# Kernel optimization log

Measured on AMD Instinct MI355X. Metric: run time of the kernel, lower is better.

Reference implementation:

```python
import jax, jax.numpy as jnp
import numpy as np

B, D, H, W, C = 2, 128, 128, 128, 4
OD, OH, OW = 96, 96, 96
RANK = 3


def setup_inputs() -> dict:
    key = jax.random.key(0)
    k1, k2 = jax.random.split(key)
    inputs = jax.random.normal(k1, (B, D, H, W, C), dtype=jnp.float32)
    # continuous sample coords in [0, size-1] per spatial dim
    scale = jnp.array([D - 1, H - 1, W - 1], dtype=jnp.float32)
    sample_coords = jax.random.uniform(k2, (B, OD, OH, OW, RANK), dtype=jnp.float32) * scale
    return {"inputs": inputs, "sample_coords": sample_coords}


def _pyramid_combination(samples, w_0, w_1):
    # recursive weighted blend over 2^rank corner samples (matches TF module)
    if len(w_0) == 1:
        return samples[0] * w_1[0] + samples[1] * w_0[0]
    f_0 = _pyramid_combination(samples[::2], w_0[:-1], w_1[:-1])
    f_1 = _pyramid_combination(samples[1::2], w_0[:-1], w_1[:-1])
    return f_0 * w_1[-1] + f_1 * w_0[-1]


def reference(inputs, sample_coords):
    # inputs: [B, D, H, W, C]; sample_coords: [B, od, oh, ow, 3]
    in_spatial = inputs.shape[1:-1]
    rank = len(in_spatial)
    batch = inputs.shape[0]

    coords = [sample_coords[..., d] for d in range(rank)]          # each [B, od, oh, ow]
    base = [jnp.floor(c) for c in coords]
    # ZERO boundary -> replicate clamp of integer coords
    floor_i = [jnp.clip(b.astype(jnp.int32), 0, in_spatial[d] - 1) for d, b in enumerate(base)]
    ceil_i = [jnp.clip((b + 1.0).astype(jnp.int32), 0, in_spatial[d] - 1) for d, b in enumerate(base)]

    # ZERO-boundary weights use the CLAMPED corner coords (faithful to source)
    w_0 = [(c - f.astype(jnp.float32))[..., None] for c, f in zip(coords, floor_i)]
    w_1 = [(ce.astype(jnp.float32) - c)[..., None] for c, ce in zip(coords, ceil_i)]

    bids = jnp.arange(batch)[:, None, None, None]                  # broadcast batch ids
    sc = (floor_i, ceil_i)

    samples = []
    for i in range(2 ** rank):
        bits = [(i >> (rank - 1 - d)) & 1 for d in range(rank)]    # dim-0 is most significant bit
        idx = [sc[bits[d]][d] for d in range(rank)]
        samples.append(inputs[bids, idx[0], idx[1], idx[2]])       # [B, od, oh, ow, C]

    return _pyramid_combination(samples, w_0, w_1)
```

## Files before the change

kernel.cpp:

```cpp
#include <hip/hip_runtime.h>
#include <hip/hip_fp16.h>


constexpr int D = 128, H = 128, W = 128;
constexpr int OD = 96, OH = 96, OW = 96;
constexpr int VOX_PER_B = OD * OH * OW;
constexpr int NVOX = 2 * VOX_PER_B;

constexpr int NBINS = 1024;
constexpr int CAP = 2048;
constexpr int NB1 = 216;
constexpr int SPB = 8192;
constexpr int GT = 1024;
constexpr int TILE_ELEMS = 9 * 5 * 128;

struct Rec { unsigned w0, w1, w2; };

constexpr size_t OFF_GCNT    = 0;
constexpr size_t OFF_RECORDS = 4096;
constexpr size_t WS_REQUIRED = OFF_RECORDS + (size_t)NBINS * CAP * 12;

__device__ __forceinline__ float4 f4_fma(float w, float4 a, float4 acc) {
    acc.x = fmaf(w, a.x, acc.x);
    acc.y = fmaf(w, a.y, acc.y);
    acc.z = fmaf(w, a.z, acc.z);
    acc.w = fmaf(w, a.w, acc.w);
    return acc;
}
__device__ __forceinline__ float4 f4_scale(float w, float4 a) {
    return make_float4(w * a.x, w * a.y, w * a.z, w * a.w);
}

__device__ __forceinline__ float4 xblend(uint2 p0, uint2 p1, float w0, float w1) {
    const __half2 a0 = *(const __half2*)&p0.x;
    const __half2 a1 = *(const __half2*)&p0.y;
    const __half2 b0 = *(const __half2*)&p1.x;
    const __half2 b1 = *(const __half2*)&p1.y;
    const float2 A0 = __half22float2(a0), A1 = __half22float2(a1);
    const float2 B0 = __half22float2(b0), B1 = __half22float2(b1);
    float4 o;
    o.x = fmaf(w1, B0.x, w0 * A0.x);
    o.y = fmaf(w1, B0.y, w0 * A0.y);
    o.z = fmaf(w1, B1.x, w0 * A1.x);
    o.w = fmaf(w1, B1.y, w0 * A1.y);
    return o;
}

__device__ __forceinline__ float4 trilinear(const float* __restrict__ inp,
                                            float cz, float cy, float cx, int b) {
    const int fz = (int)floorf(cz);
    const int fy = (int)floorf(cy);
    const int fx = (int)floorf(cx);
    const int z1 = min(max(fz + 1, 0), D - 1);
    const int y1 = min(max(fy + 1, 0), H - 1);
    const int x1 = min(max(fx + 1, 0), W - 1);
    const int z0 = min(max(fz, 0), D - 1);
    const int y0 = min(max(fy, 0), H - 1);
    const int x0 = min(max(fx, 0), W - 1);
    const float wz0 = (float)z1 - cz, wz1 = cz - (float)z0;
    const float wy0 = (float)y1 - cy, wy1 = cy - (float)y0;
    const float wx0 = (float)x1 - cx, wx1 = cx - (float)x0;
    const float4* bp = (const float4*)inp + ((size_t)b << 21);
    const int z0o = z0 << 14, z1o = z1 << 14;
    const int y0o = y0 << 7,  y1o = y1 << 7;
    const float4 s000 = bp[z0o | y0o | x0];
    const float4 s001 = bp[z0o | y0o | x1];
    const float4 s010 = bp[z0o | y1o | x0];
    const float4 s011 = bp[z0o | y1o | x1];
    const float4 s100 = bp[z1o | y0o | x0];
    const float4 s101 = bp[z1o | y0o | x1];
    const float4 s110 = bp[z1o | y1o | x0];
    const float4 s111 = bp[z1o | y1o | x1];
    float4 c00 = f4_fma(wx1, s001, f4_scale(wx0, s000));
    float4 c01 = f4_fma(wx1, s011, f4_scale(wx0, s010));
    float4 c10 = f4_fma(wx1, s101, f4_scale(wx0, s100));
    float4 c11 = f4_fma(wx1, s111, f4_scale(wx0, s110));
    float4 c0 = f4_fma(wy1, c01, f4_scale(wy0, c00));
    float4 c1 = f4_fma(wy1, c11, f4_scale(wy0, c10));
    return f4_fma(wz1, c1, f4_scale(wz0, c0));
}

__global__ __launch_bounds__(1024) void fused_scatter_kernel(
    const float* __restrict__ coords,
    const float* __restrict__ inp,
    unsigned* __restrict__ gcnt,
    Rec* __restrict__ records,
    float4* __restrict__ out)
{
    __shared__ Rec rec[SPB];
    __shared__ unsigned short binid[SPB];
    __shared__ unsigned cnt[NBINS];
    __shared__ unsigned pref[NBINS];
    __shared__ unsigned gb[NBINS];
    __shared__ unsigned s[1024];
    const int t = threadIdx.x;
    cnt[t] = 0;
    __syncthreads();

    const int s0 = blockIdx.x * SPB;
    unsigned w0r[8], w1r[8], w2r[8], rankr[8];
    int kr[8];
#pragma unroll
    for (int j = 0; j < 8; j++) {
        const int smp = s0 + j * 1024 + t;
        const float cz = coords[smp * 3 + 0];
        const float cy = coords[smp * 3 + 1];
        const float cx = coords[smp * 3 + 2];
        const int b = (smp >= VOX_PER_B) ? 1 : 0;
        const int z0 = (int)floorf(cz);
        const int y0 = (int)floorf(cy);
        const int x0 = (int)floorf(cx);
        const unsigned fzq = min((unsigned)((cz - (float)z0) * 65536.0f), 65535u);
        const unsigned fyq = min((unsigned)((cy - (float)y0) * 65536.0f), 65535u);
        const unsigned fxq = min((unsigned)((cx - (float)x0) * 65536.0f), 65535u);
        const int k = (b << 9) | ((z0 >> 3) << 5) | (y0 >> 2);
        kr[j] = k;
        w0r[j] = (unsigned)smp | ((unsigned)(z0 & 7) << 21) | ((unsigned)(y0 & 3) << 24);
        w1r[j] = fzq | (fyq << 16);
        w2r[j] = fxq | ((unsigned)x0 << 16);
        rankr[j] = atomicAdd(&cnt[k], 1u);
    }
    __syncthreads();

    pref[t] = cnt[t];
    __syncthreads();
    for (int off = 1; off < NBINS; off <<= 1) {
        unsigned u = (t >= off) ? pref[t - off] : 0u;
        __syncthreads();
        pref[t] += u;
        __syncthreads();
    }
    {
        unsigned ex = pref[t] - cnt[t];
        __syncthreads();
        pref[t] = ex;
    }
    gb[t] = atomicAdd(&gcnt[t], cnt[t]);
    __syncthreads();

#pragma unroll
    for (int j = 0; j < 8; j++) {
        const unsigned slot = pref[kr[j]] + rankr[j];
        rec[slot].w0 = w0r[j];
        rec[slot].w1 = w1r[j];
        rec[slot].w2 = w2r[j];
        binid[slot] = (unsigned short)kr[j];
    }
    __syncthreads();

#pragma unroll
    for (int j = 0; j < 8; j++) {
        const int i = j * 1024 + t;
        const int k = binid[i];
        const unsigned pos = gb[k] + (unsigned)(i - (int)pref[k]);
        const Rec r = rec[i];
        if (pos < (unsigned)CAP) {
            records[(size_t)k * CAP + pos] = r;
        } else {
            const unsigned idx = r.w0 & 0x1FFFFFu;
            const int b  = k >> 9;
            const int z0 = ((k >> 5) & 15) * 8 + (int)((r.w0 >> 21) & 7u);
            const int y0 = (k & 31) * 4 + (int)((r.w0 >> 24) & 3u);
            const int x0 = (int)(r.w2 >> 16) & 127;
            const float cz = (float)z0 + (float)(r.w1 & 0xFFFFu) * (1.0f / 65536.0f);
            const float cy = (float)y0 + (float)(r.w1 >> 16) * (1.0f / 65536.0f);
            const float cx = (float)x0 + (float)(r.w2 & 0xFFFFu) * (1.0f / 65536.0f);
            out[idx] = trilinear(inp, cz, cy, cx, b);
        }
    }
}

__device__ __forceinline__ void blend_store(const uint2* __restrict__ tile,
                                            const Rec r, float4* __restrict__ out) {
    const unsigned idx = r.w0 & 0x1FFFFFu;
    const int z0l = (int)((r.w0 >> 21) & 7u);
    const int y0l = (int)((r.w0 >> 24) & 3u);
    const int x0  = (int)(r.w2 >> 16) & 127;
    const float wz1 = (float)(r.w1 & 0xFFFFu) * (1.0f / 65536.0f);
    const float wy1 = (float)(r.w1 >> 16) * (1.0f / 65536.0f);
    const float wx1 = (float)(r.w2 & 0xFFFFu) * (1.0f / 65536.0f);
    const float wz0 = 1.0f - wz1, wy0 = 1.0f - wy1, wx0 = 1.0f - wx1;

    const int a00 = z0l * 640 + y0l * 128 + x0;
    const int a01 = a00 + 128;
    const int a10 = a00 + 640;
    const int a11 = a00 + 768;

    const float4 c00 = xblend(tile[a00], tile[a00 + 1], wx0, wx1);
    const float4 c01 = xblend(tile[a01], tile[a01 + 1], wx0, wx1);
    const float4 c10 = xblend(tile[a10], tile[a10 + 1], wx0, wx1);
    const float4 c11 = xblend(tile[a11], tile[a11 + 1], wx0, wx1);

    const float4 c0 = f4_fma(wy1, c01, f4_scale(wy0, c00));
    const float4 c1 = f4_fma(wy1, c11, f4_scale(wy0, c10));
    out[idx] = f4_fma(wz1, c1, f4_scale(wz0, c0));
}

__global__ __launch_bounds__(GT, 8) void gather_kernel(
    const float* __restrict__ inp,
    const Rec* __restrict__ records,
    const unsigned* __restrict__ gcnt,
    float4* __restrict__ out)
{
    __shared__ uint2 tile[TILE_ELEMS];
    const int k = ((blockIdx.x & 7) << 7) | (blockIdx.x >> 3);
    const int b  = k >> 9;
    const int zb = (k >> 5) & 15;
    const int yb = k & 31;
    const int t = threadIdx.x;

    const Rec* rbase = records + (size_t)k * CAP;
    const Rec r0 = rbase[t];
    const Rec r1 = rbase[t + GT];
    const unsigned n = min(gcnt[k], (unsigned)CAP);

    const float4* bp = (const float4*)inp + ((size_t)b << 21);
    const int z8 = zb * 8, y4 = yb * 4;
#pragma unroll
    for (int j = 0; j < 6; j++) {
        const int i = j * GT + t;
        if (j < 5 || i < TILE_ELEMS) {
            const int z = i / 640;
            const int rr = i - z * 640;
            const int y = rr >> 7;
            const int x = rr & 127;
            const int zg = min(z8 + z, D - 1);
            const int yg = min(y4 + y, H - 1);
            const float4 v = bp[(zg << 14) | (yg << 7) | x];
            const __half2 lo = __floats2half2_rn(v.x, v.y);
            const __half2 hi = __floats2half2_rn(v.z, v.w);
            tile[i] = make_uint2(*(const unsigned*)&lo, *(const unsigned*)&hi);
        }
    }
    __syncthreads();

    if ((unsigned)t < n)      blend_store(tile, r0, out);
    if ((unsigned)t + GT < n) blend_store(tile, r1, out);
}

__global__ __launch_bounds__(256) void direct_kernel(const float* __restrict__ inp,
                                                     const float* __restrict__ coords,
                                                     float4* __restrict__ out) {
    const int idx = blockIdx.x * 256 + threadIdx.x;
    if (idx >= NVOX) return;
    const float cz = coords[idx * 3 + 0];
    const float cy = coords[idx * 3 + 1];
    const float cx = coords[idx * 3 + 2];
    const int b = (idx >= VOX_PER_B) ? 1 : 0;
    out[idx] = trilinear(inp, cz, cy, cx, b);
}

extern "C" void kernel_launch(void* const* d_in, const int* in_sizes, int n_in,
                              void* d_out, int out_size, void* d_ws, size_t ws_size,
                              hipStream_t stream) {
    const float* inp    = (const float*)d_in[0];
    const float* coords = (const float*)d_in[1];
    float4* out = (float4*)d_out;

    if (ws_size < WS_REQUIRED) {
        direct_kernel<<<(NVOX + 255) / 256, 256, 0, stream>>>(inp, coords, out);
        return;
    }

    char* ws = (char*)d_ws;
    unsigned* gcnt    = (unsigned*)(ws + OFF_GCNT);
    Rec*      records = (Rec*)(ws + OFF_RECORDS);

    hipMemsetAsync(gcnt, 0, NBINS * sizeof(unsigned), stream);
    fused_scatter_kernel<<<NB1, 1024, 0, stream>>>(coords, inp, gcnt, records, out);
    gather_kernel<<<NBINS, GT, 0, stream>>>(inp, records, gcnt, out);
}
```

Before: 159.7 us.

## Use wave-shuffle prefix scan, nontemporal record/output traffic, and batched tile reads

Replaces the block-wide shared-memory Hillis-Steele scan in the scatter kernel with a two-level wave-shuffle scan, removing about 20 barriers. Record writes and reads, and the final output stores, now use nontemporal builtins to reduce cache pollution. The gather kernel issues all 16 LDS tile reads for both records up front, unconditionally, before blending, so the loads can overlap. It pads the tile by 2 elements so that out-of-range garbage records cannot read past the tile, at the cost of wasted work on empty slots.

```diff
diff --git a/kernel.cpp b/kernel.cpp
--- a/kernel.cpp
+++ b/kernel.cpp
@@ -14,6 +14,8 @@
 constexpr int GT = 1024;
 constexpr int TILE_ELEMS = 9 * 5 * 128;
 
+typedef float floatx4 __attribute__((ext_vector_type(4)));
+
 struct Rec { unsigned w0, w1, w2; };
 
 constexpr size_t OFF_GCNT    = 0;
@@ -29,6 +31,11 @@
 }
 __device__ __forceinline__ float4 f4_scale(float w, float4 a) {
     return make_float4(w * a.x, w * a.y, w * a.z, w * a.w);
+}
+__device__ __forceinline__ void nt_store_f4(float4 v, float4* p) {
+    floatx4 nv;
+    nv.x = v.x; nv.y = v.y; nv.z = v.z; nv.w = v.w;
+    __builtin_nontemporal_store(nv, (floatx4*)p);
 }
 
 __device__ __forceinline__ float4 xblend(uint2 p0, uint2 p1, float w0, float w1) {
@@ -92,7 +99,7 @@
     __shared__ unsigned cnt[NBINS];
     __shared__ unsigned pref[NBINS];
     __shared__ unsigned gb[NBINS];
-    __shared__ unsigned s[1024];
+    __shared__ unsigned wsum[16];
     const int t = threadIdx.x;
     cnt[t] = 0;
     __syncthreads();
@@ -122,20 +129,28 @@
     }
     __syncthreads();
 
-    pref[t] = cnt[t];
-    __syncthreads();
-    for (int off = 1; off < NBINS; off <<= 1) {
-        unsigned u = (t >= off) ? pref[t - off] : 0u;
-        __syncthreads();
-        pref[t] += u;
-        __syncthreads();
-    }
-    {
-        unsigned ex = pref[t] - cnt[t];
-        __syncthreads();
-        pref[t] = ex;
-    }
-    gb[t] = atomicAdd(&gcnt[t], cnt[t]);
+    const unsigned cv = cnt[t];
+    unsigned x = cv;
+#pragma unroll
+    for (int off = 1; off < 64; off <<= 1) {
+        const unsigned u = __shfl_up(x, (unsigned)off, 64);
+        if ((t & 63) >= off) x += u;
+    }
+    if ((t & 63) == 63) wsum[t >> 6] = x;
+    __syncthreads();
+    if (t < 16) {
+        const unsigned wv = wsum[t];
+        unsigned xx = wv;
+#pragma unroll
+        for (int off = 1; off < 16; off <<= 1) {
+            const unsigned u = __shfl_up(xx, (unsigned)off, 64);
+            if (t >= off) xx += u;
+        }
+        wsum[t] = xx - wv;
+    }
+    __syncthreads();
+    pref[t] = wsum[t >> 6] + (x - cv);
+    gb[t] = atomicAdd(&gcnt[t], cv);
     __syncthreads();
 
 #pragma unroll
@@ -155,7 +170,10 @@
         const unsigned pos = gb[k] + (unsigned)(i - (int)pref[k]);
         const Rec r = rec[i];
         if (pos < (unsigned)CAP) {
-            records[(size_t)k * CAP + pos] = r;
+            unsigned* p = &records[(size_t)k * CAP + pos].w0;
+            __builtin_nontemporal_store(r.w0, p + 0);
+            __builtin_nontemporal_store(r.w1, p + 1);
+            __builtin_nontemporal_store(r.w2, p + 2);
         } else {
             const unsigned idx = r.w0 & 0x1FFFFFu;
             const int b  = k >> 9;
@@ -170,48 +188,27 @@
     }
 }
 
-__device__ __forceinline__ void blend_store(const uint2* __restrict__ tile,
-                                            const Rec r, float4* __restrict__ out) {
-    const unsigned idx = r.w0 & 0x1FFFFFu;
-    const int z0l = (int)((r.w0 >> 21) & 7u);
-    const int y0l = (int)((r.w0 >> 24) & 3u);
-    const int x0  = (int)(r.w2 >> 16) & 127;
-    const float wz1 = (float)(r.w1 & 0xFFFFu) * (1.0f / 65536.0f);
-    const float wy1 = (float)(r.w1 >> 16) * (1.0f / 65536.0f);
-    const float wx1 = (float)(r.w2 & 0xFFFFu) * (1.0f / 65536.0f);
-    const float wz0 = 1.0f - wz1, wy0 = 1.0f - wy1, wx0 = 1.0f - wx1;
-
-    const int a00 = z0l * 640 + y0l * 128 + x0;
-    const int a01 = a00 + 128;
-    const int a10 = a00 + 640;
-    const int a11 = a00 + 768;
-
-    const float4 c00 = xblend(tile[a00], tile[a00 + 1], wx0, wx1);
-    const float4 c01 = xblend(tile[a01], tile[a01 + 1], wx0, wx1);
-    const float4 c10 = xblend(tile[a10], tile[a10 + 1], wx0, wx1);
-    const float4 c11 = xblend(tile[a11], tile[a11 + 1], wx0, wx1);
-
-    const float4 c0 = f4_fma(wy1, c01, f4_scale(wy0, c00));
-    const float4 c1 = f4_fma(wy1, c11, f4_scale(wy0, c10));
-    out[idx] = f4_fma(wz1, c1, f4_scale(wz0, c0));
-}
-
 __global__ __launch_bounds__(GT, 8) void gather_kernel(
     const float* __restrict__ inp,
     const Rec* __restrict__ records,
     const unsigned* __restrict__ gcnt,
     float4* __restrict__ out)
 {
-    __shared__ uint2 tile[TILE_ELEMS];
+    __shared__ uint2 tile[TILE_ELEMS + 2];
     const int k = ((blockIdx.x & 7) << 7) | (blockIdx.x >> 3);
     const int b  = k >> 9;
     const int zb = (k >> 5) & 15;
     const int yb = k & 31;
     const int t = threadIdx.x;
 
-    const Rec* rbase = records + (size_t)k * CAP;
-    const Rec r0 = rbase[t];
-    const Rec r1 = rbase[t + GT];
+    const unsigned* rp0 = &records[(size_t)k * CAP + t].w0;
+    const unsigned r0w0 = __builtin_nontemporal_load(rp0 + 0);
+    const unsigned r0w1 = __builtin_nontemporal_load(rp0 + 1);
+    const unsigned r0w2 = __builtin_nontemporal_load(rp0 + 2);
+    const unsigned* rp1 = rp0 + (size_t)GT * 3;
+    const unsigned r1w0 = __builtin_nontemporal_load(rp1 + 0);
+    const unsigned r1w1 = __builtin_nontemporal_load(rp1 + 1);
+    const unsigned r1w2 = __builtin_nontemporal_load(rp1 + 2);
     const unsigned n = min(gcnt[k], (unsigned)CAP);
 
     const float4* bp = (const float4*)inp + ((size_t)b << 21);
@@ -234,8 +231,50 @@
     }
     __syncthreads();
 
-    if ((unsigned)t < n)      blend_store(tile, r0, out);
-    if ((unsigned)t + GT < n) blend_store(tile, r1, out);
+    const int a0 = (int)((r0w0 >> 21) & 7u) * 640 + (int)((r0w0 >> 24) & 3u) * 128
+                 + ((int)(r0w2 >> 16) & 127);
+    const int a1 = (int)((r1w0 >> 21) & 7u) * 640 + (int)((r1w0 >> 24) & 3u) * 128
+                 + ((int)(r1w2 >> 16) & 127);
+
+    const uint2 p000 = tile[a0],       p001 = tile[a0 + 1];
+    const uint2 p010 = tile[a0 + 128], p011 = tile[a0 + 129];
+    const uint2 p100 = tile[a0 + 640], p101 = tile[a0 + 641];
+    const uint2 p110 = tile[a0 + 768], p111 = tile[a0 + 769];
+    const uint2 q000 = tile[a1],       q001 = tile[a1 + 1];
+    const uint2 q010 = tile[a1 + 128], q011 = tile[a1 + 129];
+    const uint2 q100 = tile[a1 + 640], q101 = tile[a1 + 641];
+    const uint2 q110 = tile[a1 + 768], q111 = tile[a1 + 769];
+
+    {
+        const float wz1 = (float)(r0w1 & 0xFFFFu) * (1.0f / 65536.0f);
+        const float wy1 = (float)(r0w1 >> 16) * (1.0f / 65536.0f);
+        const float wx1 = (float)(r0w2 & 0xFFFFu) * (1.0f / 65536.0f);
+        const float wz0 = 1.0f - wz1, wy0 = 1.0f - wy1, wx0 = 1.0f - wx1;
+        const float4 c00 = xblend(p000, p001, wx0, wx1);
+        const float4 c01 = xblend(p010, p011, wx0, wx1);
+        const float4 c10 = xblend(p100, p101, wx0, wx1);
+        const float4 c11 = xblend(p110, p111, wx0, wx1);
+        const float4 c0 = f4_fma(wy1, c01, f4_scale(wy0, c00));
+        const float4 c1 = f4_fma(wy1, c11, f4_scale(wy0, c10));
+        const float4 v = f4_fma(wz1, c1, f4_scale(wz0, c0));
+        if ((unsigned)t < n)
+            nt_store_f4(v, &out[r0w0 & 0x1FFFFFu]);
+    }
+    {
+        const float wz1 = (float)(r1w1 & 0xFFFFu) * (1.0f / 65536.0f);
+        const float wy1 = (float)(r1w1 >> 16) * (1.0f / 65536.0f);
+        const float wx1 = (float)(r1w2 & 0xFFFFu) * (1.0f / 65536.0f);
+        const float wz0 = 1.0f - wz1, wy0 = 1.0f - wy1, wx0 = 1.0f - wx1;
+        const float4 c00 = xblend(q000, q001, wx0, wx1);
+        const float4 c01 = xblend(q010, q011, wx0, wx1);
+        const float4 c10 = xblend(q100, q101, wx0, wx1);
+        const float4 c11 = xblend(q110, q111, wx0, wx1);
+        const float4 c0 = f4_fma(wy1, c01, f4_scale(wy0, c00));
+        const float4 c1 = f4_fma(wy1, c11, f4_scale(wy0, c10));
+        const float4 v = f4_fma(wz1, c1, f4_scale(wz0, c0));
+        if ((unsigned)t + GT < n)
+            nt_store_f4(v, &out[r1w0 & 0x1FFFFFu]);
+    }
 }
 
 __global__ __launch_bounds__(256) void direct_kernel(const float* __restrict__ inp,
```

New measurement: 196.5 us. 23.0% more time.
